# Kernel optimization log

Measured on AMD Instinct MI355X. Metric: run time of the kernel, lower is better.

## Reference

```python
import jax, jax.numpy as jnp
import numpy as np

DX, DU = 4, 2   # dim_x, dim_u of the linear-Gaussian env
P = 8192        # num_p particles (also number of backward samples)
LOG_2PI = float(np.log(2.0 * np.pi))


def setup_inputs() -> dict:
    key = jax.random.key(0)
    ks = jax.random.split(key, 6)
    particles = jax.random.normal(ks[0], (P, DX + DU), dtype=jnp.float32)      # [x, u] per particle
    samples = jax.random.normal(ks[1], (P, DX), dtype=jnp.float32)             # next-step backward samples
    weights = 0.1 * jax.random.normal(ks[2], (P,), dtype=jnp.float32)          # incoming smoothed log-weights
    log_weights = jax.nn.log_softmax(jax.random.normal(ks[3], (P,), dtype=jnp.float32))  # forward filter log-weights
    A = 0.3 * jax.random.normal(ks[4], (DX, DX), dtype=jnp.float32)            # dynamics matrix
    B = 0.3 * jax.random.normal(ks[5], (DX, DU), dtype=jnp.float32)            # control matrix
    log_sigma = jnp.zeros((DX,), dtype=jnp.float32)                            # log std of dynamics noise
    return {"particles": particles, "samples": samples, "weights": weights,
            "log_weights": log_weights, "A": A, "B": B, "log_sigma": log_sigma}


def reference(particles, samples, weights, log_weights, A, B, log_sigma):
    # Vectorized ParticleI2cCell.backward_smoothing (Doucet et al. backward reweighing).
    dx = A.shape[0]
    x = particles[:, :dx]              # [P, dx]
    u = particles[:, dx:]              # [P, du]
    mean = x @ A.T + u @ B.T           # env dynamics mean, [P, dx]

    # Diagonal-Gaussian log-likelihood of every sample under every particle's
    # predicted next-state distribution, via the expanded squared distance so
    # we never materialize a [P, N, dx] tensor.
    inv_sigma = jnp.exp(-log_sigma)
    s = samples[:, :dx] * inv_sigma    # [N, dx] scaled
    m = mean * inv_sigma               # [P, dx] scaled
    sq = (jnp.sum(s * s, axis=-1)[None, :]
          + jnp.sum(m * m, axis=-1)[:, None]
          - 2.0 * (m @ s.T))           # [P, N] squared Mahalanobis distance
    ll = -0.5 * sq - jnp.sum(log_sigma) - 0.5 * dx * LOG_2PI  # [P, N]

    # forward_ll_norm = logsumexp(forward_ll + self.log_weights) per particle
    norm = jax.scipy.special.logsumexp(ll + log_weights[None, :], axis=1)      # [P]
    # smoothed_weights[p] = logsumexp(forward_ll + weights - norm)
    smoothed = jax.scipy.special.logsumexp(ll + weights[None, :] - norm[:, None], axis=1)  # [P]
    return smoothed
```

## Files before the change

kernel.cpp:

```cpp
#include <hip/hip_runtime.h>


constexpr float LOG2E = 1.4426950408889634f;
constexpr float LN2   = 0.6931471805599453f;

__global__ __launch_bounds__(256) void precompute_k(
    const float* __restrict__ particles,
    const float* __restrict__ samples,
    const float* __restrict__ weights,
    const float* __restrict__ log_weights,
    const float* __restrict__ A,
    const float* __restrict__ B,
    const float* __restrict__ log_sigma,
    float* __restrict__ jdata,
    float* __restrict__ msoa,
    int P)
{
    int i = blockIdx.x * blockDim.x + threadIdx.x;
    if (i >= P) return;

    const float K = -0.5f * LOG2E;

    float inv_s[4];
#pragma unroll
    for (int k = 0; k < 4; ++k)
        inv_s[k] = __builtin_amdgcn_exp2f(-log_sigma[k] * LOG2E);

    float4 sv = reinterpret_cast<const float4*>(samples)[i];
    float s0 = sv.x * inv_s[0], s1 = sv.y * inv_s[1];
    float s2 = sv.z * inv_s[2], s3 = sv.w * inv_s[3];
    float sn = s0*s0 + s1*s1 + s2*s2 + s3*s3;

    float4* jd = reinterpret_cast<float4*>(jdata + (size_t)i * 8);
    jd[0] = make_float4(LOG2E*s0, LOG2E*s1, LOG2E*s2, LOG2E*s3);
    jd[1] = make_float4(K * sn,
                        __builtin_amdgcn_exp2f(log_weights[i] * LOG2E),
                        __builtin_amdgcn_exp2f(weights[i] * LOG2E),
                        0.f);

    const float2* p2 = reinterpret_cast<const float2*>(particles) + (size_t)i * 3;
    float2 x01 = p2[0], x23 = p2[1], u01 = p2[2];
    float x[4] = {x01.x, x01.y, x23.x, x23.y};
    float u[2] = {u01.x, u01.y};
#pragma unroll
    for (int k = 0; k < 4; ++k) {
        float mean =       A[k*4+0] * x[0];
        mean = fmaf(A[k*4+1], x[1], mean);
        mean = fmaf(A[k*4+2], x[2], mean);
        mean = fmaf(A[k*4+3], x[3], mean);
        mean = fmaf(B[k*2+0], u[0], mean);
        mean = fmaf(B[k*2+1], u[1], mean);
        msoa[(size_t)k * P + i] = mean * inv_s[k];
    }
}

template <int TR, int BLOCK>
__global__ __launch_bounds__(BLOCK, 4) void pair_fused(
    const float* __restrict__ jdata,
    const float* __restrict__ msoa,
    float* __restrict__ out, int P)
{
    constexpr int NW = BLOCK / 64;

    const int tid  = threadIdx.x;
    const int lane = tid & 63;
    const int wv   = tid >> 6;
    const int rowBase = blockIdx.x * TR;

    float m0[TR], m1[TR], m2[TR], m3[TR], a1[TR], a2[TR];
#pragma unroll
    for (int r = 0; r < TR; ++r) {
        m0[r] = msoa[0 * (size_t)P + rowBase + r];
        m1[r] = msoa[1 * (size_t)P + rowBase + r];
        m2[r] = msoa[2 * (size_t)P + rowBase + r];
        m3[r] = msoa[3 * (size_t)P + rowBase + r];
        a1[r] = 0.f;
        a2[r] = 0.f;
    }

    const float4* jf = reinterpret_cast<const float4*>(jdata);
    const int iters = P / BLOCK;
#pragma unroll 4
    for (int it = 0; it < iters; ++it) {
        const int j = it * BLOCK + tid;
        float4 av = jf[2 * j];
        float4 bv = jf[2 * j + 1];
#pragma unroll
        for (int r = 0; r < TR; ++r) {
            float t = fmaf(m0[r], av.x, bv.x);
            t = fmaf(m1[r], av.y, t);
            t = fmaf(m2[r], av.z, t);
            t = fmaf(m3[r], av.w, t);
            float e = __builtin_amdgcn_exp2f(t);
            a1[r] = fmaf(e, bv.y, a1[r]);
            a2[r] = fmaf(e, bv.z, a2[r]);
        }
    }

#pragma unroll
    for (int r = 0; r < TR; ++r) {
#pragma unroll
        for (int mask = 32; mask >= 1; mask >>= 1) {
            a1[r] += __shfl_xor(a1[r], mask, 64);
            a2[r] += __shfl_xor(a2[r], mask, 64);
        }
    }

    __shared__ float red[NW][2 * TR];
    if (lane == 0) {
#pragma unroll
        for (int r = 0; r < TR; ++r) {
            red[wv][r]      = a1[r];
            red[wv][TR + r] = a2[r];
        }
    }
    __syncthreads();
    if (tid < TR) {
        float s1 = 0.f, s2 = 0.f;
#pragma unroll
        for (int w = 0; w < NW; ++w) {
            s1 += red[w][tid];
            s2 += red[w][TR + tid];
        }
        out[rowBase + tid] =
            (__builtin_amdgcn_logf(s2) - __builtin_amdgcn_logf(s1)) * LN2;
    }
}

extern "C" void kernel_launch(void* const* d_in, const int* in_sizes, int n_in,
                              void* d_out, int out_size, void* d_ws, size_t ws_size,
                              hipStream_t stream)
{
    const float* particles   = (const float*)d_in[0];
    const float* samples     = (const float*)d_in[1];
    const float* weights     = (const float*)d_in[2];
    const float* log_weights = (const float*)d_in[3];
    const float* A           = (const float*)d_in[4];
    const float* B           = (const float*)d_in[5];
    const float* log_sigma   = (const float*)d_in[6];

    const int P = in_sizes[2];

    float* jdata = (float*)d_ws;
    float* msoa  = jdata + (size_t)P * 8;

    constexpr int BLOCK = 256, TR = 8;

    precompute_k<<<(P + BLOCK - 1) / BLOCK, BLOCK, 0, stream>>>(
        particles, samples, weights, log_weights, A, B, log_sigma,
        jdata, msoa, P);

    pair_fused<TR, BLOCK><<<P / TR, BLOCK, 0, stream>>>(
        jdata, msoa, (float*)d_out, P);
}
```

Measured before the change: 27.04 us.

## Split pairwise reduction over sample halves with separate combine kernel

The pairwise kernel now splits the sample (j) dimension into two chunks over a 2D grid. Each block writes partial sums to workspace, and a new combine kernel adds the partials and takes the log-ratio. Row means are loaded through readfirstlane so they sit in scalar registers, and the occupancy hint rises to 8. This is meant to double the number of blocks and cut vector register pressure to improve latency hiding. It costs an extra kernel launch and a round trip of partial sums through memory.

```diff
diff --git a/kernel.cpp b/kernel.cpp
--- a/kernel.cpp
+++ b/kernel.cpp
@@ -54,32 +54,37 @@
     }
 }
 
-template <int TR, int BLOCK>
-__global__ __launch_bounds__(BLOCK, 4) void pair_fused(
+template <int TR, int BLOCK, int NSPLIT>
+__global__ __launch_bounds__(BLOCK, 8) void pair_half(
     const float* __restrict__ jdata,
     const float* __restrict__ msoa,
-    float* __restrict__ out, int P)
+    float* __restrict__ part1,
+    float* __restrict__ part2,
+    int P)
 {
     constexpr int NW = BLOCK / 64;
 
     const int tid  = threadIdx.x;
     const int lane = tid & 63;
     const int wv   = tid >> 6;
-    const int rowBase = blockIdx.x * TR;
+    const int jc   = blockIdx.x;
+    const int rowBase = blockIdx.y * TR;
 
     float m0[TR], m1[TR], m2[TR], m3[TR], a1[TR], a2[TR];
 #pragma unroll
     for (int r = 0; r < TR; ++r) {
-        m0[r] = msoa[0 * (size_t)P + rowBase + r];
-        m1[r] = msoa[1 * (size_t)P + rowBase + r];
-        m2[r] = msoa[2 * (size_t)P + rowBase + r];
-        m3[r] = msoa[3 * (size_t)P + rowBase + r];
+        m0[r] = __builtin_amdgcn_readfirstlane(msoa[0 * (size_t)P + rowBase + r]);
+        m1[r] = __builtin_amdgcn_readfirstlane(msoa[1 * (size_t)P + rowBase + r]);
+        m2[r] = __builtin_amdgcn_readfirstlane(msoa[2 * (size_t)P + rowBase + r]);
+        m3[r] = __builtin_amdgcn_readfirstlane(msoa[3 * (size_t)P + rowBase + r]);
         a1[r] = 0.f;
         a2[r] = 0.f;
     }
 
-    const float4* jf = reinterpret_cast<const float4*>(jdata);
-    const int iters = P / BLOCK;
+    const int jspan = P / NSPLIT;
+    const float4* jf = reinterpret_cast<const float4*>(jdata) +
+                       (size_t)jc * jspan * 2;
+    const int iters = jspan / BLOCK;
 #pragma unroll 4
     for (int it = 0; it < iters; ++it) {
         const int j = it * BLOCK + tid;
@@ -122,9 +127,26 @@
             s1 += red[w][tid];
             s2 += red[w][TR + tid];
         }
-        out[rowBase + tid] =
-            (__builtin_amdgcn_logf(s2) - __builtin_amdgcn_logf(s1)) * LN2;
+        part1[(size_t)jc * P + rowBase + tid] = s1;
+        part2[(size_t)jc * P + rowBase + tid] = s2;
     }
+}
+
+template <int NSPLIT>
+__global__ __launch_bounds__(256) void combine_k(
+    const float* __restrict__ part1,
+    const float* __restrict__ part2,
+    float* __restrict__ out, int P)
+{
+    int i = blockIdx.x * blockDim.x + threadIdx.x;
+    if (i >= P) return;
+    float s1 = 0.f, s2 = 0.f;
+#pragma unroll
+    for (int c = 0; c < NSPLIT; ++c) {
+        s1 += part1[(size_t)c * P + i];
+        s2 += part2[(size_t)c * P + i];
+    }
+    out[i] = (__builtin_amdgcn_logf(s2) - __builtin_amdgcn_logf(s1)) * LN2;
 }
 
 extern "C" void kernel_launch(void* const* d_in, const int* in_sizes, int n_in,
@@ -141,15 +163,21 @@
 
     const int P = in_sizes[2];
 
+    constexpr int BLOCK = 256, TR = 8, NSPLIT = 2;
+
     float* jdata = (float*)d_ws;
     float* msoa  = jdata + (size_t)P * 8;
+    float* part1 = msoa + (size_t)P * 4;
+    float* part2 = part1 + (size_t)NSPLIT * P;
 
-    constexpr int BLOCK = 256, TR = 8;
-
-    precompute_k<<<(P + BLOCK - 1) / BLOCK, BLOCK, 0, stream>>>(
+    precompute_k<<<(P + 255) / 256, 256, 0, stream>>>(
         particles, samples, weights, log_weights, A, B, log_sigma,
         jdata, msoa, P);
 
-    pair_fused<TR, BLOCK><<<P / TR, BLOCK, 0, stream>>>(
-        jdata, msoa, (float*)d_out, P);
+    dim3 grid(NSPLIT, P / TR);
+    pair_half<TR, BLOCK, NSPLIT><<<grid, BLOCK, 0, stream>>>(
+        jdata, msoa, part1, part2, P);
+
+    combine_k<NSPLIT><<<(P + 255) / 256, 256, 0, stream>>>(
+        part1, part2, (float*)d_out, P);
 }
```

Result: slower. 32.15 us (+18.9%).

## Fuse precompute into pair kernel, recomputing sample terms per block

Applied to the files above, without the earlier changes.

Removes the separate precompute kernel and workspace buffers. Each block now derives its particle means from the raw inputs and recomputes per-sample norms and the exp of both weight vectors inside the inner loop. Folding the sigma scaling into the means lets the raw samples be used directly. This saves one launch and the workspace round trip, at the cost of redundant per-sample exp2 and FMA work repeated by every one of the 1024 blocks.

```diff
diff --git a/kernel.cpp b/kernel.cpp
--- a/kernel.cpp
+++ b/kernel.cpp
@@ -4,7 +4,8 @@
 constexpr float LOG2E = 1.4426950408889634f;
 constexpr float LN2   = 0.6931471805599453f;
 
-__global__ __launch_bounds__(256) void precompute_k(
+template <int TR, int BLOCK>
+__global__ __launch_bounds__(BLOCK, 4) void fused_all(
     const float* __restrict__ particles,
     const float* __restrict__ samples,
     const float* __restrict__ weights,
@@ -12,52 +13,6 @@
     const float* __restrict__ A,
     const float* __restrict__ B,
     const float* __restrict__ log_sigma,
-    float* __restrict__ jdata,
-    float* __restrict__ msoa,
-    int P)
-{
-    int i = blockIdx.x * blockDim.x + threadIdx.x;
-    if (i >= P) return;
-
-    const float K = -0.5f * LOG2E;
-
-    float inv_s[4];
-#pragma unroll
-    for (int k = 0; k < 4; ++k)
-        inv_s[k] = __builtin_amdgcn_exp2f(-log_sigma[k] * LOG2E);
-
-    float4 sv = reinterpret_cast<const float4*>(samples)[i];
-    float s0 = sv.x * inv_s[0], s1 = sv.y * inv_s[1];
-    float s2 = sv.z * inv_s[2], s3 = sv.w * inv_s[3];
-    float sn = s0*s0 + s1*s1 + s2*s2 + s3*s3;
-
-    float4* jd = reinterpret_cast<float4*>(jdata + (size_t)i * 8);
-    jd[0] = make_float4(LOG2E*s0, LOG2E*s1, LOG2E*s2, LOG2E*s3);
-    jd[1] = make_float4(K * sn,
-                        __builtin_amdgcn_exp2f(log_weights[i] * LOG2E),
-                        __builtin_amdgcn_exp2f(weights[i] * LOG2E),
-                        0.f);
-
-    const float2* p2 = reinterpret_cast<const float2*>(particles) + (size_t)i * 3;
-    float2 x01 = p2[0], x23 = p2[1], u01 = p2[2];
-    float x[4] = {x01.x, x01.y, x23.x, x23.y};
-    float u[2] = {u01.x, u01.y};
-#pragma unroll
-    for (int k = 0; k < 4; ++k) {
-        float mean =       A[k*4+0] * x[0];
-        mean = fmaf(A[k*4+1], x[1], mean);
-        mean = fmaf(A[k*4+2], x[2], mean);
-        mean = fmaf(A[k*4+3], x[3], mean);
-        mean = fmaf(B[k*2+0], u[0], mean);
-        mean = fmaf(B[k*2+1], u[1], mean);
-        msoa[(size_t)k * P + i] = mean * inv_s[k];
-    }
-}
-
-template <int TR, int BLOCK>
-__global__ __launch_bounds__(BLOCK, 4) void pair_fused(
-    const float* __restrict__ jdata,
-    const float* __restrict__ msoa,
     float* __restrict__ out, int P)
 {
     constexpr int NW = BLOCK / 64;
@@ -67,33 +22,59 @@
     const int wv   = tid >> 6;
     const int rowBase = blockIdx.x * TR;
 
-    float m0[TR], m1[TR], m2[TR], m3[TR], a1[TR], a2[TR];
+    float inv2[4], Kinv[4];
+#pragma unroll
+    for (int k = 0; k < 4; ++k) {
+        float iv = __builtin_amdgcn_exp2f(-log_sigma[k] * LOG2E);
+        inv2[k] = iv * iv;
+        Kinv[k] = -0.5f * LOG2E * inv2[k];
+    }
+
+    float M0[TR], M1[TR], M2[TR], M3[TR], a1[TR], a2[TR];
 #pragma unroll
     for (int r = 0; r < TR; ++r) {
-        m0[r] = msoa[0 * (size_t)P + rowBase + r];
-        m1[r] = msoa[1 * (size_t)P + rowBase + r];
-        m2[r] = msoa[2 * (size_t)P + rowBase + r];
-        m3[r] = msoa[3 * (size_t)P + rowBase + r];
+        const float* pr = particles + (size_t)(rowBase + r) * 6;
+        float x0 = pr[0], x1 = pr[1], x2 = pr[2], x3 = pr[3];
+        float u0 = pr[4], u1 = pr[5];
+        float mk[4];
+#pragma unroll
+        for (int k = 0; k < 4; ++k) {
+            float mean =       A[k*4+0] * x0;
+            mean = fmaf(A[k*4+1], x1, mean);
+            mean = fmaf(A[k*4+2], x2, mean);
+            mean = fmaf(A[k*4+3], x3, mean);
+            mean = fmaf(B[k*2+0], u0, mean);
+            mean = fmaf(B[k*2+1], u1, mean);
+            mk[k] = LOG2E * mean * inv2[k];
+        }
+        M0[r] = mk[0]; M1[r] = mk[1]; M2[r] = mk[2]; M3[r] = mk[3];
         a1[r] = 0.f;
         a2[r] = 0.f;
     }
 
-    const float4* jf = reinterpret_cast<const float4*>(jdata);
+    const float4* sf = reinterpret_cast<const float4*>(samples);
     const int iters = P / BLOCK;
 #pragma unroll 4
     for (int it = 0; it < iters; ++it) {
         const int j = it * BLOCK + tid;
-        float4 av = jf[2 * j];
-        float4 bv = jf[2 * j + 1];
+        float4 sv = sf[j];
+        float w  = weights[j];
+        float lw = log_weights[j];
+        float cn = Kinv[0] * sv.x * sv.x;
+        cn = fmaf(Kinv[1] * sv.y, sv.y, cn);
+        cn = fmaf(Kinv[2] * sv.z, sv.z, cn);
+        cn = fmaf(Kinv[3] * sv.w, sv.w, cn);
+        float elw = __builtin_amdgcn_exp2f(lw * LOG2E);
+        float ew  = __builtin_amdgcn_exp2f(w * LOG2E);
 #pragma unroll
         for (int r = 0; r < TR; ++r) {
-            float t = fmaf(m0[r], av.x, bv.x);
-            t = fmaf(m1[r], av.y, t);
-            t = fmaf(m2[r], av.z, t);
-            t = fmaf(m3[r], av.w, t);
+            float t = fmaf(M0[r], sv.x, cn);
+            t = fmaf(M1[r], sv.y, t);
+            t = fmaf(M2[r], sv.z, t);
+            t = fmaf(M3[r], sv.w, t);
             float e = __builtin_amdgcn_exp2f(t);
-            a1[r] = fmaf(e, bv.y, a1[r]);
-            a2[r] = fmaf(e, bv.z, a2[r]);
+            a1[r] = fmaf(e, elw, a1[r]);
+            a2[r] = fmaf(e, ew,  a2[r]);
         }
     }
 
@@ -141,15 +122,9 @@
 
     const int P = in_sizes[2];
 
-    float* jdata = (float*)d_ws;
-    float* msoa  = jdata + (size_t)P * 8;
-
     constexpr int BLOCK = 256, TR = 8;
 
-    precompute_k<<<(P + BLOCK - 1) / BLOCK, BLOCK, 0, stream>>>(
+    fused_all<TR, BLOCK><<<P / TR, BLOCK, 0, stream>>>(
         particles, samples, weights, log_weights, A, B, log_sigma,
-        jdata, msoa, P);
-
-    pair_fused<TR, BLOCK><<<P / TR, BLOCK, 0, stream>>>(
-        jdata, msoa, (float*)d_out, P);
+        (float*)d_out, P);
 }
```

After: 27.05 us. Within noise of the previous version (+0.0%).
